# Optimization experiments

Measured on AMD Instinct MI355X. Metric: run time of the kernel, lower is better.

The kernel has to match this reference:

```python
import jax, jax.numpy as jnp
import numpy as np

NUM_FEATURES = 20480
NUM_ACCUMULATORS = 128


def setup_inputs() -> dict:
    key = jax.random.key(0)
    k1, k2, k3, k4, k5, k6 = jax.random.split(key, 6)
    B = 4096
    white = jax.random.uniform(k1, (B, NUM_FEATURES), dtype=jnp.float32)
    black = jax.random.uniform(k2, (B, NUM_FEATURES), dtype=jnp.float32)
    # learned params (torch nn.Linear stores weight as [out, in])
    w_psqt = jax.random.normal(k3, (2, NUM_FEATURES), dtype=jnp.float32) * 0.01
    w_acc = jax.random.normal(k4, (NUM_ACCUMULATORS, NUM_FEATURES), dtype=jnp.float32) * 0.01
    b_acc = jax.random.normal(k5, (NUM_ACCUMULATORS,), dtype=jnp.float32) * 0.01
    w_layer = jax.random.normal(k6, (2, NUM_ACCUMULATORS), dtype=jnp.float32) * 0.1
    return {"white": white, "black": black, "w_psqt": w_psqt,
            "w_acc": w_acc, "b_acc": b_acc, "w_layer": w_layer}


def reference(white, black, w_psqt, w_acc, b_acc, w_layer):
    # psqt: Linear(NUM_FEATURES -> 2, no bias)
    psqt = jnp.einsum('bf,of->bo', white, w_psqt) - jnp.einsum('bf,of->bo', black, w_psqt)
    # accumulator: Linear(NUM_FEATURES -> 128) + CReLU clamp(0, 1)
    white_acc = jnp.clip(jnp.einsum('bf,af->ba', white, w_acc) + b_acc, 0.0, 1.0)
    black_acc = jnp.clip(jnp.einsum('bf,af->ba', black, w_acc) + b_acc, 0.0, 1.0)
    # output layer: Linear(128 -> 2, no bias)
    positional = jnp.einsum('ba,oa->bo', white_acc, w_layer) - jnp.einsum('ba,oa->bo', black_acc, w_layer)
    return psqt + positional
```

## Files before the change

### kernel.cpp

```cpp
#include <hip/hip_runtime.h>
#include <hip/hip_bf16.h>
#include <stdint.h>

typedef __attribute__((ext_vector_type(4))) float          f32x4;
typedef __attribute__((ext_vector_type(8))) short          short8;
typedef __attribute__((ext_vector_type(4))) unsigned short u16x4;

#define F            20480
#define NROWS        4096
#define NPAD         144
#define BK           128
#define CHUNK_BYTES  (NPAD * BK * 2)
#define TOTAL_CHUNKS (F / BK)
#define MB           256

static __device__ __forceinline__ unsigned short f2bf(float f) {
    unsigned u = __builtin_bit_cast(unsigned, f);
    unsigned r = (u + 0x7FFFu + ((u >> 16) & 1u)) >> 16;
    return (unsigned short)r;
}

__global__ __launch_bounds__(256) void prep_b(const float* __restrict__ w_acc,
                                              const float* __restrict__ w_psqt,
                                              unsigned short* __restrict__ Bp) {
    int gid = blockIdx.x * 256 + threadIdx.x;
    int p8    = gid * 8;
    int chunk = p8 / CHUNK_BYTES;
    int win   = p8 % CHUNK_BYTES;
    int n     = win >> 8;
    int sb    = win & 255;
    int kbyte = sb ^ ((n & 7) << 4);
    int k0    = chunk * BK + (kbyte >> 1);
    f32x4 v = {0.f, 0.f, 0.f, 0.f};
    if (n < 128)      v = *(const f32x4*)(w_acc  + (size_t)n * F + k0);
    else if (n < 130) v = *(const f32x4*)(w_psqt + (size_t)(n - 128) * F + k0);
    u16x4 pk;
    pk[0] = f2bf(v[0]); pk[1] = f2bf(v[1]); pk[2] = f2bf(v[2]); pk[3] = f2bf(v[3]);
    *(u16x4*)((char*)Bp + p8) = pk;
}

__global__ __launch_bounds__(512, 2) void gemm_main(
    const float* __restrict__ white, const float* __restrict__ black,
    const unsigned short* __restrict__ Bp, _Float16* __restrict__ partial,
    int chunks_per_ks)
{
    __shared__ alignas(16) unsigned short Blds[2][CHUNK_BYTES / 2];

    const int tid  = threadIdx.x;
    const int wave = tid >> 6;
    const int lane = tid & 63;
    const int g    = lane >> 4;
    const int r16  = lane & 15;

    const int rg   = blockIdx.x;
    const int row0 = rg * MB;
    const float* Aside = (row0 < NROWS) ? white : black;
    const int arow0 = row0 & (NROWS - 1);

    const int chunk0 = blockIdx.y * chunks_per_ks;
    const int nch    = chunks_per_ks;

    const float* aRow0 = Aside + (size_t)(arow0 + wave * 32 + r16) * F + g * 8;
    const float* aRow1 = aRow0 + (size_t)16 * F;

    f32x4 apf[2][4][2];
    f32x4 acc[2][9];
    const f32x4 zero = {0.f, 0.f, 0.f, 0.f};
    #pragma unroll
    for (int m = 0; m < 2; ++m)
        #pragma unroll
        for (int n = 0; n < 9; ++n) acc[m][n] = zero;

    auto stageB = [&](int buf, int chunk) {
        const char* src = (const char*)Bp + (size_t)chunk * CHUNK_BYTES + lane * 16;
        char* dst = (char*)(&Blds[buf][0]);
        #pragma unroll
        for (int line = 0; line < 5; ++line) {
            int li = wave + line * 8;
            if (li < 36)
                __builtin_amdgcn_global_load_lds(
                    (const __attribute__((address_space(1))) void*)(src + li * 1024),
                    (__attribute__((address_space(3))) void*)(dst + li * 1024),
                    16, 0, 0);
        }
    };

    auto loadA = [&](int kbase) {
        #pragma unroll
        for (int m = 0; m < 2; ++m) {
            const float* p = (m ? aRow1 : aRow0) + kbase;
            #pragma unroll
            for (int kk = 0; kk < 4; ++kk) {
                apf[m][kk][0] = *(const f32x4*)(p + kk * 32);
                apf[m][kk][1] = *(const f32x4*)(p + kk * 32 + 4);
            }
        }
    };

    stageB(0, chunk0);
    loadA(chunk0 * BK);

    for (int t = 0; t < nch; ++t) {
        __syncthreads();

        short8 afr[2][4];
        #pragma unroll
        for (int m = 0; m < 2; ++m)
            #pragma unroll
            for (int kk = 0; kk < 4; ++kk) {
                short8 r;
                #pragma unroll
                for (int j = 0; j < 4; ++j) {
                    r[j]     = (short)f2bf(apf[m][kk][0][j]);
                    r[j + 4] = (short)f2bf(apf[m][kk][1][j]);
                }
                afr[m][kk] = r;
            }

        if (t + 1 < nch) {
            stageB((t + 1) & 1, chunk0 + t + 1);
            loadA((chunk0 + t + 1) * BK);
        }

        const char* bb = (const char*)(&Blds[t & 1][0]);
        #pragma unroll
        for (int kk = 0; kk < 4; ++kk) {
            #pragma unroll
            for (int n = 0; n < 9; ++n) {
                const int nn  = n * 16 + r16;
                const int off = nn * 256 + ((kk * 64 + g * 16) ^ ((nn & 7) << 4));
                short8 bf = *(const short8*)(bb + off);
                acc[0][n] = __builtin_amdgcn_mfma_f32_16x16x32_bf16(afr[0][kk], bf, acc[0][n], 0, 0, 0);
                acc[1][n] = __builtin_amdgcn_mfma_f32_16x16x32_bf16(afr[1][kk], bf, acc[1][n], 0, 0, 0);
            }
        }
    }

    _Float16* prow = partial + ((size_t)blockIdx.y * 8192 + row0 + wave * 32 + g * 4) * NPAD;
    #pragma unroll
    for (int m = 0; m < 2; ++m)
        #pragma unroll
        for (int n = 0; n < 9; ++n)
            #pragma unroll
            for (int j = 0; j < 4; ++j)
                prow[(m * 16 + j) * NPAD + n * 16 + r16] = (_Float16)acc[m][n][j];
}

__global__ __launch_bounds__(256) void epilogue(
    const _Float16* __restrict__ partial, const float* __restrict__ b_acc,
    const float* __restrict__ w_layer, float* __restrict__ out, int KS)
{
    const int wave = threadIdx.x >> 6, lane = threadIdx.x & 63;
    const int b = blockIdx.x * 4 + wave;
    float sw0 = 0, sw1 = 0, sb0 = 0, sb1 = 0, q0 = 0, q1 = 0;
    for (int ks = 0; ks < KS; ++ks) {
        const _Float16* Pw = partial + ((size_t)ks * 8192 + b) * NPAD;
        const _Float16* Pb = partial + ((size_t)ks * 8192 + NROWS + b) * NPAD;
        sw0 += (float)Pw[lane];      sw1 += (float)Pw[lane + 64];
        sb0 += (float)Pb[lane];      sb1 += (float)Pb[lane + 64];
        q0  += (float)Pw[128] - (float)Pb[128];
        q1  += (float)Pw[129] - (float)Pb[129];
    }
    float wa0 = fminf(fmaxf(sw0 + b_acc[lane], 0.f), 1.f);
    float wa1 = fminf(fmaxf(sw1 + b_acc[lane + 64], 0.f), 1.f);
    float ba0 = fminf(fmaxf(sb0 + b_acc[lane], 0.f), 1.f);
    float ba1 = fminf(fmaxf(sb1 + b_acc[lane + 64], 0.f), 1.f);
    float d0 = wa0 - ba0, d1 = wa1 - ba1;
    float p0 = w_layer[lane] * d0       + w_layer[lane + 64] * d1;
    float p1 = w_layer[128 + lane] * d0 + w_layer[192 + lane] * d1;
    #pragma unroll
    for (int off = 32; off >= 1; off >>= 1) {
        p0 += __shfl_xor(p0, off, 64);
        p1 += __shfl_xor(p1, off, 64);
    }
    if (lane == 0) {
        out[b * 2 + 0] = q0 + p0;
        out[b * 2 + 1] = q1 + p1;
    }
}

extern "C" void kernel_launch(void* const* d_in, const int* in_sizes, int n_in,
                              void* d_out, int out_size, void* d_ws, size_t ws_size,
                              hipStream_t stream)
{
    const float* white   = (const float*)d_in[0];
    const float* black   = (const float*)d_in[1];
    const float* w_psqt  = (const float*)d_in[2];
    const float* w_acc   = (const float*)d_in[3];
    const float* b_acc   = (const float*)d_in[4];
    const float* w_layer = (const float*)d_in[5];
    float* out = (float*)d_out;

    const size_t bbytes = (size_t)TOTAL_CHUNKS * CHUNK_BYTES;
    unsigned short* Bp = (unsigned short*)d_ws;
    _Float16* partial = (_Float16*)((char*)d_ws + bbytes);

    const size_t per_ks = (size_t)8192 * NPAD * 2;
    int KS = 1;
    const int cands[5] = {8, 5, 4, 2, 1};
    for (int i = 0; i < 5; ++i)
        if (bbytes + (size_t)cands[i] * per_ks <= ws_size) { KS = cands[i]; break; }
    int chunks_per_ks = TOTAL_CHUNKS / KS;

    prep_b   <<<dim3(2880),   dim3(256), 0, stream>>>(w_acc, w_psqt, Bp);
    gemm_main<<<dim3(32, KS), dim3(512), 0, stream>>>(white, black, Bp, partial, chunks_per_ks);
    epilogue <<<dim3(1024),   dim3(256), 0, stream>>>(partial, b_acc, w_layer, out, KS);
}
```

Baseline: 149.1 us.

## Double K chunk to 256 and split A prefetch into two halves

Raises the K-chunk size from 128 to 256, so each barrier and B stage into LDS covers twice the work, and the prep kernel's swizzled layout is adjusted to match. Each chunk is now processed in two halves: the A registers for the second half are loaded while the first half runs its MFMAs, and the next chunk's first half is prefetched during the second half. The aim is to cut barrier overhead and better overlap global A loads with matrix math. In exchange, the double-buffered LDS footprint doubles to about 147 KB, which probably allows only one block per CU instead of two.

```diff
diff --git a/kernel.cpp b/kernel.cpp
--- a/kernel.cpp
+++ b/kernel.cpp
@@ -9,7 +9,7 @@
 #define F            20480
 #define NROWS        4096
 #define NPAD         144
-#define BK           128
+#define BK           256
 #define CHUNK_BYTES  (NPAD * BK * 2)
 #define TOTAL_CHUNKS (F / BK)
 #define MB           256
@@ -27,8 +27,8 @@
     int p8    = gid * 8;
     int chunk = p8 / CHUNK_BYTES;
     int win   = p8 % CHUNK_BYTES;
-    int n     = win >> 8;
-    int sb    = win & 255;
+    int n     = win >> 9;
+    int sb    = win & 511;
     int kbyte = sb ^ ((n & 7) << 4);
     int k0    = chunk * BK + (kbyte >> 1);
     f32x4 v = {0.f, 0.f, 0.f, 0.f};
@@ -75,20 +75,19 @@
         const char* src = (const char*)Bp + (size_t)chunk * CHUNK_BYTES + lane * 16;
         char* dst = (char*)(&Blds[buf][0]);
         #pragma unroll
-        for (int line = 0; line < 5; ++line) {
+        for (int line = 0; line < 9; ++line) {
             int li = wave + line * 8;
-            if (li < 36)
-                __builtin_amdgcn_global_load_lds(
-                    (const __attribute__((address_space(1))) void*)(src + li * 1024),
-                    (__attribute__((address_space(3))) void*)(dst + li * 1024),
-                    16, 0, 0);
+            __builtin_amdgcn_global_load_lds(
+                (const __attribute__((address_space(1))) void*)(src + li * 1024),
+                (__attribute__((address_space(3))) void*)(dst + li * 1024),
+                16, 0, 0);
         }
     };
 
-    auto loadA = [&](int kbase) {
+    auto loadA = [&](int kbase, int h) {
         #pragma unroll
         for (int m = 0; m < 2; ++m) {
-            const float* p = (m ? aRow1 : aRow0) + kbase;
+            const float* p = (m ? aRow1 : aRow0) + kbase + h * 128;
             #pragma unroll
             for (int kk = 0; kk < 4; ++kk) {
                 apf[m][kk][0] = *(const f32x4*)(p + kk * 32);
@@ -97,13 +96,8 @@
         }
     };
 
-    stageB(0, chunk0);
-    loadA(chunk0 * BK);
-
-    for (int t = 0; t < nch; ++t) {
-        __syncthreads();
-
-        short8 afr[2][4];
+    short8 afr0[2][4], afr1[2][4];
+    auto cvtA = [&](short8 (&afr)[2][4]) {
         #pragma unroll
         for (int m = 0; m < 2; ++m)
             #pragma unroll
@@ -116,11 +110,18 @@
                 }
                 afr[m][kk] = r;
             }
-
-        if (t + 1 < nch) {
+    };
+
+    stageB(0, chunk0);
+    loadA(chunk0 * BK, 0);
+
+    for (int t = 0; t < nch; ++t) {
+        __syncthreads();
+
+        cvtA(afr0);
+        loadA((chunk0 + t) * BK, 1);
+        if (t + 1 < nch)
             stageB((t + 1) & 1, chunk0 + t + 1);
-            loadA((chunk0 + t + 1) * BK);
-        }
 
         const char* bb = (const char*)(&Blds[t & 1][0]);
         #pragma unroll
@@ -128,10 +129,26 @@
             #pragma unroll
             for (int n = 0; n < 9; ++n) {
                 const int nn  = n * 16 + r16;
-                const int off = nn * 256 + ((kk * 64 + g * 16) ^ ((nn & 7) << 4));
+                const int off = nn * 512 + ((kk * 64 + g * 16) ^ ((nn & 7) << 4));
                 short8 bf = *(const short8*)(bb + off);
-                acc[0][n] = __builtin_amdgcn_mfma_f32_16x16x32_bf16(afr[0][kk], bf, acc[0][n], 0, 0, 0);
-                acc[1][n] = __builtin_amdgcn_mfma_f32_16x16x32_bf16(afr[1][kk], bf, acc[1][n], 0, 0, 0);
+                acc[0][n] = __builtin_amdgcn_mfma_f32_16x16x32_bf16(afr0[0][kk], bf, acc[0][n], 0, 0, 0);
+                acc[1][n] = __builtin_amdgcn_mfma_f32_16x16x32_bf16(afr0[1][kk], bf, acc[1][n], 0, 0, 0);
+            }
+        }
+
+        cvtA(afr1);
+        if (t + 1 < nch)
+            loadA((chunk0 + t + 1) * BK, 0);
+
+        #pragma unroll
+        for (int kk = 0; kk < 4; ++kk) {
+            #pragma unroll
+            for (int n = 0; n < 9; ++n) {
+                const int nn  = n * 16 + r16;
+                const int off = nn * 512 + (((kk + 4) * 64 + g * 16) ^ ((nn & 7) << 4));
+                short8 bf = *(const short8*)(bb + off);
+                acc[0][n] = __builtin_amdgcn_mfma_f32_16x16x32_bf16(afr1[0][kk], bf, acc[0][n], 0, 0, 0);
+                acc[1][n] = __builtin_amdgcn_mfma_f32_16x16x32_bf16(afr1[1][kk], bf, acc[1][n], 0, 0, 0);
             }
         }
     }
```

Result: no change. 147.4 us (-1.1%).
